# Performance work log

Measured on AMD Instinct MI355X. Metric: run time of the kernel, lower is better.

Reference implementation:

```python
import jax, jax.numpy as jnp
import numpy as np


def conv1x1(x, w, b):
    # x: [B,C,H,W], w: [O,C], b: [O]
    return jnp.einsum('bchw,oc->bohw', x, w) + b[None, :, None, None]


def dwconv(x, w):
    # depthwise conv, x: [B,C,H,W], w: [C,1,k,k], SAME padding (k odd, pad=k//2)
    return jax.lax.conv_general_dilated(
        x, w, window_strides=(1, 1), padding='SAME',
        dimension_numbers=('NCHW', 'OIHW', 'NCHW'),
        feature_group_count=x.shape[1])


def setup_inputs() -> dict:
    key = jax.random.key(0)
    ks = jax.random.split(key, 14)
    B, C, H, W = 16, 256, 64, 64
    OC = C // 16  # scale=16 -> 16
    WSCALE = 0.05
    r = lambda k, shape: jax.random.normal(k, shape, dtype=jnp.float32) * WSCALE
    return {
        'x': jax.random.normal(ks[0], (B, C, H, W), dtype=jnp.float32),
        'conv_w': r(ks[1], (C + 4, C)),           # 1x1 conv -> ctx (C) + gates (3+1)
        'conv_b': r(ks[2], (C + 4,)),
        'fw3': r(ks[3], (C, 1, 3, 3)),            # depthwise focal kernels
        'fw5': r(ks[4], (C, 1, 5, 5)),
        'fw7': r(ks[5], (C, 1, 7, 7)),
        'key_w': r(ks[6], (1, C)),                # Conv_key 1x1
        'key_b': r(ks[7], (1,)),
        'v1_w': r(ks[8], (OC, C)),                # Conv_value first 1x1
        'v1_b': r(ks[9], (OC,)),
        'ln_w': jnp.ones((OC,), dtype=jnp.float32),
        'ln_b': jnp.zeros((OC,), dtype=jnp.float32),
        'v2_w': r(ks[10], (C, OC)),               # Conv_value second 1x1
        'v2_b': r(ks[11], (C,)),
    }


def reference(x, conv_w, conv_b, fw3, fw5, fw7, key_w, key_b,
              v1_w, v1_b, ln_w, ln_b, v2_w, v2_b):
    B, C, H, W = x.shape
    # _contextAggregation
    t = conv1x1(x, conv_w, conv_b)          # [B, C+4, H, W]
    ctx, gates = t[:, :C], t[:, C:]         # [B,C,H,W], [B,4,H,W]
    ctx_all = jnp.zeros_like(ctx)
    for l, fw in enumerate((fw3, fw5, fw7)):
        ctx = jax.nn.gelu(dwconv(ctx, fw), approximate=False)  # torch GELU = exact erf
        ctx_all = ctx_all + ctx * gates[:, l:l + 1]
    ctx_global = jnp.mean(ctx, axis=(2, 3), keepdims=True)     # AdaptiveAvgPool2d(1)
    ctx_all = ctx_all + ctx_global * gates[:, 3:4]
    # GC-style channel attention: softmax over spatial positions
    k = conv1x1(ctx_all, key_w, key_b).reshape(B, H * W)       # [B, HW]
    k = jax.nn.softmax(k, axis=1)
    q = ctx_all.reshape(B, C, H * W)
    qk = jnp.einsum('bcn,bn->bc', q, k)[:, :, None, None]      # [B,C,1,1]
    # Conv_value: 1x1 -> LayerNorm([OC,1,1]) -> ReLU -> 1x1
    v = conv1x1(qk, v1_w, v1_b)                                # [B,OC,1,1]
    mu = jnp.mean(v, axis=(1, 2, 3), keepdims=True)
    var = jnp.var(v, axis=(1, 2, 3), keepdims=True)
    v = (v - mu) * jax.lax.rsqrt(var + 1e-5)
    v = v * ln_w[None, :, None, None] + ln_b[None, :, None, None]
    v = jax.nn.relu(v)
    v = conv1x1(v, v2_w, v2_b)                                 # [B,C,1,1]
    return ctx_all + v
```

## Files before the change

kernel.cpp:

```cpp
#include <hip/hip_runtime.h>

#define DEVFN __device__ __forceinline__

constexpr int B  = 16;
constexpr int C  = 256;
constexpr int N  = 64 * 64;
constexpr int O1 = C + 4;

typedef __attribute__((ext_vector_type(8)))  short bf16x8;
typedef __attribute__((ext_vector_type(4)))  short bf16x4;
typedef __attribute__((ext_vector_type(16))) float f32x16;
typedef unsigned short ushort_t;

DEVFN short f2bf(float f){
  union { float f; unsigned u; } p; p.f = f;
  unsigned r = p.u + 0x7fffu + ((p.u >> 16) & 1u);
  return (short)(r >> 16);
}
DEVFN unsigned pack2(float lo, float hi){
  return (unsigned)(ushort_t)f2bf(lo) | ((unsigned)(ushort_t)f2bf(hi) << 16);
}
DEVFN float lo2f(unsigned u){ union{unsigned u; float f;} p; p.u = u << 16; return p.f; }
DEVFN float hi2f(unsigned u){ union{unsigned u; float f;} p; p.u = u & 0xffff0000u; return p.f; }
DEVFN float bf2f(ushort_t s){ union{unsigned u; float f;} p; p.u = (unsigned)s << 16; return p.f; }

DEVFN float gelu_fast(float x){
  float y = 1.5957691216f * fmaf(0.044715f * x * x, x, x);
  float s = __builtin_amdgcn_rcpf(1.0f + __expf(-y));
  return x * s;
}

__global__ __launch_bounds__(256)
void k_wbf(const float* __restrict__ w, ushort_t* __restrict__ wbf){
  int idx = blockIdx.x * 256 + threadIdx.x;
  int o = idx >> 8, cc = idx & 255;
  wbf[idx] = (o < O1) ? (ushort_t)f2bf(w[o * 256 + cc]) : (ushort_t)0;
}

__global__ __launch_bounds__(256, 3)
void k_conv1_mfma(const float* __restrict__ x, const ushort_t* __restrict__ wbf,
                  const float* __restrict__ bias, ushort_t* __restrict__ ctxb,
                  float* __restrict__ gates){
  __shared__ __align__(16) short wlds[8 * 320 * 8];
  __shared__ __align__(16) short xlds[8 * 64 * 8];
  __shared__ float sbias[320];
  const int tid  = threadIdx.x;
  const int wave = tid >> 6;
  const int lane = tid & 63;
  const int l31  = lane & 31;
  const int lhi  = lane >> 5;
  const int pg0  = blockIdx.x * 64;
  const int b    = pg0 >> 12;
  const int n0   = pg0 & 4095;
  const int nwv  = (wave & 1) * 32;
  const int mrow = wave >> 1;

  sbias[tid] = bias[tid];
  if(tid < 64) sbias[256 + tid] = (256 + tid < O1) ? bias[256 + tid] : 0.f;

  const float* xpb = x + (size_t)b * C * N + n0;

  f32x16 acc[5];
  #pragma unroll
  for(int t = 0; t < 5; t++)
    #pragma unroll
    for(int r = 0; r < 16; r++) acc[t][r] = 0.f;

  float xf[2][8];

  auto pfX = [&](int kc){
    #pragma unroll
    for(int p = 0; p < 2; p++){
      const int idx = p * 256 + tid;
      const int kg = idx >> 6, n = idx & 63;
      const float* xp = xpb + (size_t)(kc + kg * 8) * N + n;
      #pragma unroll
      for(int j = 0; j < 8; j++) xf[p][j] = xp[(size_t)j * N];
    }
  };
  auto stX = [&](){
    #pragma unroll
    for(int p = 0; p < 2; p++){
      const int idx = p * 256 + tid;
      const int kg = idx >> 6, n = idx & 63;
      uint4 v;
      v.x = pack2(xf[p][0], xf[p][1]); v.y = pack2(xf[p][2], xf[p][3]);
      v.z = pack2(xf[p][4], xf[p][5]); v.w = pack2(xf[p][6], xf[p][7]);
      *(uint4*)&xlds[(kg * 64 + n) * 8] = v;
    }
  };
  auto stW = [&](int kc){
    #pragma unroll
    for(int q = 0; q < 10; q++){
      const int pidx = q * 256 + tid;
      const int kg = pidx / 320;
      const int m  = pidx - kg * 320;
      uint4 v = *(const uint4*)(wbf + (size_t)m * 256 + kc + kg * 8);
      *(uint4*)&wlds[(kg * 320 + m) * 8] = v;
    }
  };
  auto mfmaC = [&](){
    #pragma unroll
    for(int ks = 0; ks < 4; ks++){
      const int kg = ks * 2 + lhi;
      bf16x8 bfr = *(const bf16x8*)&xlds[(kg * 64 + nwv + l31) * 8];
      #pragma unroll
      for(int t = 0; t < 5; t++){
        const int m0 = (mrow + 2 * t) * 32;
        bf16x8 af = *(const bf16x8*)&wlds[(kg * 320 + m0 + l31) * 8];
        acc[t] = __builtin_amdgcn_mfma_f32_32x32x16_bf16(af, bfr, acc[t], 0, 0, 0);
      }
    }
  };

  stW(0); pfX(0); stX();
  __syncthreads();
  pfX(64);
  mfmaC();
  __syncthreads();
  stW(64); stX();
  __syncthreads();
  pfX(128);
  mfmaC();
  __syncthreads();
  stW(128); stX();
  __syncthreads();
  pfX(192);
  mfmaC();
  __syncthreads();
  stW(192); stX();
  __syncthreads();
  mfmaC();

  const int n = n0 + nwv + l31;
  #pragma unroll
  for(int t = 0; t < 5; t++){
    const int mt = (mrow + 2 * t) * 32;
    #pragma unroll
    for(int r = 0; r < 16; r++){
      const int row = (r & 3) + 8 * (r >> 2) + 4 * lhi;
      const int o = mt + row;
      if(o >= O1) continue;
      const float v = acc[t][r] + sbias[o];
      if(o < 256)
        ctxb[((size_t)(b * 256 + o)) * N + n] = (ushort_t)f2bf(v);
      else
        gates[((size_t)(b * 4 + (o - 256))) * N + n] = v;
    }
  }
}

constexpr int SSTR = 72;

DEVFN void unpack16(const short* p, float* wnd){
  uint4 a = *(const uint4*)p;
  uint4 b = *(const uint4*)(p + 8);
  unsigned ua[8] = {a.x, a.y, a.z, a.w, b.x, b.y, b.z, b.w};
  #pragma unroll
  for(int d = 0; d < 8; d++){ wnd[2*d] = lo2f(ua[d]); wnd[2*d+1] = hi2f(ua[d]); }
}

template<int K>
DEVFN void dw_stage(const short* src, const float* __restrict__ fw, int c,
                    int h, int w0, float* val){
  constexpr int R = K / 2;
  float acc[8];
  #pragma unroll
  for(int i = 0; i < 8; i++) acc[i] = 0.f;
  #pragma unroll
  for(int ky = 0; ky < K; ky++){
    const int r = h + ky - R;
    if((unsigned)r < 64u){
      float wnd[16];
      unpack16(&src[r * SSTR + w0], wnd);
      #pragma unroll
      for(int kx = 0; kx < K; kx++){
        const float wv = fw[c * K * K + ky * K + kx];
        #pragma unroll
        for(int i = 0; i < 8; i++)
          acc[i] = fmaf(wnd[i + kx + 4 - R], wv, acc[i]);
      }
    }
  }
  #pragma unroll
  for(int i = 0; i < 8; i++) val[i] = gelu_fast(acc[i]);
}

DEVFN void store_row(short* dst, int h, int w0, const float* val){
  bf16x4 lo, hi;
  #pragma unroll
  for(int i = 0; i < 4; i++){ lo[i] = f2bf(val[i]); hi[i] = f2bf(val[i + 4]); }
  *(bf16x4*)&dst[h * SSTR + w0 + 4] = lo;
  *(bf16x4*)&dst[h * SSTR + w0 + 8] = hi;
}

__global__ __launch_bounds__(512, 8)
void k_dwchain(ushort_t* __restrict__ ctxb, const float* __restrict__ fw3,
               const float* __restrict__ fw5, const float* __restrict__ fw7,
               const float* __restrict__ gates){
  __shared__ __align__(16) short bufA[64 * SSTR];
  __shared__ __align__(16) short bufB[64 * SSTR];
  __shared__ float wred[8];
  const int tid = threadIdx.x;
  const int plane = blockIdx.x;
  const int b = plane >> 8;
  const int c = plane & 255;
  const int h  = tid >> 3;
  const int w0 = (tid & 7) * 8;
  const int nbase = h * 64 + w0;

  if(tid < 64){
    bf16x4 z = {0, 0, 0, 0};
    *(bf16x4*)&bufA[tid * SSTR] = z;  *(bf16x4*)&bufA[tid * SSTR + 68] = z;
    *(bf16x4*)&bufB[tid * SSTR] = z;  *(bf16x4*)&bufB[tid * SSTR + 68] = z;
  }
  {
    bf16x8 iv = *(const bf16x8*)((const short*)ctxb + (size_t)plane * N + tid * 8);
    bf16x4 lo, hi;
    #pragma unroll
    for(int j = 0; j < 4; j++){ lo[j] = iv[j]; hi[j] = iv[j + 4]; }
    *(bf16x4*)&bufA[h * SSTR + w0 + 4] = lo;
    *(bf16x4*)&bufA[h * SSTR + w0 + 8] = hi;
  }
  __syncthreads();

  float ctxp[8];
  #pragma unroll
  for(int i = 0; i < 8; i++) ctxp[i] = 0.f;
  float val[8];

  dw_stage<3>(bufA, fw3, c, h, w0, val);
  {
    const float* gp = gates + ((size_t)(b * 4 + 0)) * N + nbase;
    float4 ga = *(const float4*)gp, gb = *(const float4*)(gp + 4);
    ctxp[0] = fmaf(val[0], ga.x, ctxp[0]); ctxp[1] = fmaf(val[1], ga.y, ctxp[1]);
    ctxp[2] = fmaf(val[2], ga.z, ctxp[2]); ctxp[3] = fmaf(val[3], ga.w, ctxp[3]);
    ctxp[4] = fmaf(val[4], gb.x, ctxp[4]); ctxp[5] = fmaf(val[5], gb.y, ctxp[5]);
    ctxp[6] = fmaf(val[6], gb.z, ctxp[6]); ctxp[7] = fmaf(val[7], gb.w, ctxp[7]);
    store_row(bufB, h, w0, val);
  }
  __syncthreads();

  dw_stage<5>(bufB, fw5, c, h, w0, val);
  {
    const float* gp = gates + ((size_t)(b * 4 + 1)) * N + nbase;
    float4 ga = *(const float4*)gp, gb = *(const float4*)(gp + 4);
    ctxp[0] = fmaf(val[0], ga.x, ctxp[0]); ctxp[1] = fmaf(val[1], ga.y, ctxp[1]);
    ctxp[2] = fmaf(val[2], ga.z, ctxp[2]); ctxp[3] = fmaf(val[3], ga.w, ctxp[3]);
    ctxp[4] = fmaf(val[4], gb.x, ctxp[4]); ctxp[5] = fmaf(val[5], gb.y, ctxp[5]);
    ctxp[6] = fmaf(val[6], gb.z, ctxp[6]); ctxp[7] = fmaf(val[7], gb.w, ctxp[7]);
    store_row(bufA, h, w0, val);
  }
  __syncthreads();

  dw_stage<7>(bufA, fw7, c, h, w0, val);
  float lsum = 0.f;
  {
    const float* gp = gates + ((size_t)(b * 4 + 2)) * N + nbase;
    float4 ga = *(const float4*)gp, gb = *(const float4*)(gp + 4);
    ctxp[0] = fmaf(val[0], ga.x, ctxp[0]); ctxp[1] = fmaf(val[1], ga.y, ctxp[1]);
    ctxp[2] = fmaf(val[2], ga.z, ctxp[2]); ctxp[3] = fmaf(val[3], ga.w, ctxp[3]);
    ctxp[4] = fmaf(val[4], gb.x, ctxp[4]); ctxp[5] = fmaf(val[5], gb.y, ctxp[5]);
    ctxp[6] = fmaf(val[6], gb.z, ctxp[6]); ctxp[7] = fmaf(val[7], gb.w, ctxp[7]);
    #pragma unroll
    for(int i = 0; i < 8; i++) lsum += val[i];
  }
  #pragma unroll
  for(int off = 32; off > 0; off >>= 1) lsum += __shfl_xor(lsum, off, 64);
  if((tid & 63) == 0) wred[tid >> 6] = lsum;
  __syncthreads();
  float mean = 0.f;
  #pragma unroll
  for(int i = 0; i < 8; i++) mean += wred[i];
  mean *= (1.0f / 4096.0f);

  {
    const float* gp = gates + ((size_t)(b * 4 + 3)) * N + nbase;
    float4 ga = *(const float4*)gp, gb = *(const float4*)(gp + 4);
    bf16x8 ov;
    ov[0] = f2bf(fmaf(mean, ga.x, ctxp[0])); ov[1] = f2bf(fmaf(mean, ga.y, ctxp[1]));
    ov[2] = f2bf(fmaf(mean, ga.z, ctxp[2])); ov[3] = f2bf(fmaf(mean, ga.w, ctxp[3]));
    ov[4] = f2bf(fmaf(mean, gb.x, ctxp[4])); ov[5] = f2bf(fmaf(mean, gb.y, ctxp[5]));
    ov[6] = f2bf(fmaf(mean, gb.z, ctxp[6])); ov[7] = f2bf(fmaf(mean, gb.w, ctxp[7]));
    *(bf16x8*)((short*)ctxb + (size_t)plane * N + nbase) = ov;
  }
}

__global__ __launch_bounds__(256)
void k_logits(const ushort_t* __restrict__ P, const float* __restrict__ key_w,
              const float* __restrict__ key_b, float* __restrict__ logits){
  __shared__ float kw[256];
  __shared__ float part[512];
  int tid = threadIdx.x;
  kw[tid] = key_w[tid];
  __syncthreads();
  int b  = blockIdx.x >> 5;
  int n0 = (blockIdx.x & 31) * 128;
  int cpart = tid >> 6, pxp = tid & 63;
  const ushort_t* pp = P + ((size_t)(b * 256 + cpart * 64)) * N + n0 + pxp * 2;
  float a0 = 0.f, a1 = 0.f;
  #pragma unroll 8
  for(int c = 0; c < 64; c++){
    unsigned u = *(const unsigned*)(pp + (size_t)c * N);
    float kwv = kw[cpart * 64 + c];
    a0 = fmaf(lo2f(u), kwv, a0);
    a1 = fmaf(hi2f(u), kwv, a1);
  }
  part[cpart * 128 + pxp * 2]     = a0;
  part[cpart * 128 + pxp * 2 + 1] = a1;
  __syncthreads();
  if(tid < 128){
    float l = part[tid] + part[128 + tid] + part[256 + tid] + part[384 + tid];
    logits[b * N + n0 + tid] = l + key_b[0];
  }
}

__global__ __launch_bounds__(1024)
void k_softmax(float* __restrict__ kbuf){
  __shared__ float wred[16];
  int b = blockIdx.x, tid = threadIdx.x;
  const int wave = tid >> 6, lane = tid & 63;
  float v[4];
  float m = -1e30f;
  #pragma unroll
  for(int i = 0; i < 4; i++){
    v[i] = kbuf[b * N + tid + i * 1024];
    m = fmaxf(m, v[i]);
  }
  #pragma unroll
  for(int off = 32; off > 0; off >>= 1) m = fmaxf(m, __shfl_xor(m, off, 64));
  if(lane == 0) wred[wave] = m;
  __syncthreads();
  float mm = -1e30f;
  #pragma unroll
  for(int i = 0; i < 16; i++) mm = fmaxf(mm, wred[i]);
  __syncthreads();
  float s = 0.f;
  #pragma unroll
  for(int i = 0; i < 4; i++){ v[i] = __expf(v[i] - mm); s += v[i]; }
  #pragma unroll
  for(int off = 32; off > 0; off >>= 1) s += __shfl_xor(s, off, 64);
  if(lane == 0) wred[wave] = s;
  __syncthreads();
  float tot = 0.f;
  #pragma unroll
  for(int i = 0; i < 16; i++) tot += wred[i];
  float inv = 1.0f / tot;
  #pragma unroll
  for(int i = 0; i < 4; i++)
    kbuf[b * N + tid + i * 1024] = v[i] * inv;
}

__global__ __launch_bounds__(256)
void k_qk(const ushort_t* __restrict__ P, const float* __restrict__ kbuf,
          float* __restrict__ qk){
  __shared__ float red[256];
  int plane = blockIdx.x, tid = threadIdx.x;
  int b = plane >> 8;
  const unsigned* pp = (const unsigned*)(P + (size_t)plane * N);
  const float2* kp = (const float2*)(kbuf + b * N);
  float acc = 0.f;
  #pragma unroll
  for(int i = 0; i < 8; i++){
    int idx = tid + i * 256;
    unsigned u = pp[idx];
    float2 kk = kp[idx];
    acc = fmaf(lo2f(u), kk.x, acc);
    acc = fmaf(hi2f(u), kk.y, acc);
  }
  red[tid] = acc; __syncthreads();
  for(int s = 128; s > 0; s >>= 1){
    if(tid < s) red[tid] += red[tid + s];
    __syncthreads();
  }
  if(tid == 0) qk[plane] = red[0];
}

__global__ __launch_bounds__(256)
void k_v(const float* __restrict__ qk, const float* __restrict__ v1w,
         const float* __restrict__ v1b, const float* __restrict__ lnw,
         const float* __restrict__ lnb, const float* __restrict__ v2w,
         const float* __restrict__ v2b, float* __restrict__ vout){
  int b = blockIdx.x, tid = threadIdx.x;
  __shared__ float qs[256];
  __shared__ float part[256];
  __shared__ float v1s[16];
  __shared__ float vr[16];
  __shared__ float stats[2];
  qs[tid] = qk[b * 256 + tid];
  __syncthreads();
  int oc = tid >> 4, ln = tid & 15;
  float p = 0.f;
  #pragma unroll
  for(int j = 0; j < 16; j++){
    int cc = ln + j * 16;
    p = fmaf(v1w[oc * 256 + cc], qs[cc], p);
  }
  part[tid] = p;
  __syncthreads();
  if(tid < 16){
    float s = v1b[tid];
    for(int j = 0; j < 16; j++) s += part[tid * 16 + j];
    v1s[tid] = s;
  }
  __syncthreads();
  if(tid == 0){
    float mu = 0.f;
    for(int i = 0; i < 16; i++) mu += v1s[i];
    mu *= (1.f / 16.f);
    float var = 0.f;
    for(int i = 0; i < 16; i++){ float d = v1s[i] - mu; var += d * d; }
    var *= (1.f / 16.f);
    stats[0] = mu; stats[1] = rsqrtf(var + 1e-5f);
  }
  __syncthreads();
  if(tid < 16){
    float vv = (v1s[tid] - stats[0]) * stats[1] * lnw[tid] + lnb[tid];
    vr[tid] = fmaxf(vv, 0.f);
  }
  __syncthreads();
  float o = v2b[tid];
  #pragma unroll
  for(int j = 0; j < 16; j++) o = fmaf(v2w[tid * 16 + j], vr[j], o);
  vout[b * 256 + tid] = o;
}

__global__ __launch_bounds__(256)
void k_final(float* __restrict__ out, const ushort_t* __restrict__ ctxb,
             const float* __restrict__ vout){
  int idx8 = blockIdx.x * 256 + threadIdx.x;
  int plane = idx8 >> 9;
  int off = (idx8 & 511) * 8;
  bf16x8 v = *(const bf16x8*)((const short*)ctxb + (size_t)plane * N + off);
  float vv = vout[plane];
  float4 o0, o1;
  o0.x = bf2f((ushort_t)v[0]) + vv; o0.y = bf2f((ushort_t)v[1]) + vv;
  o0.z = bf2f((ushort_t)v[2]) + vv; o0.w = bf2f((ushort_t)v[3]) + vv;
  o1.x = bf2f((ushort_t)v[4]) + vv; o1.y = bf2f((ushort_t)v[5]) + vv;
  o1.z = bf2f((ushort_t)v[6]) + vv; o1.w = bf2f((ushort_t)v[7]) + vv;
  float* op = out + (size_t)plane * N + off;
  *(float4*)op = o0;
  *(float4*)(op + 4) = o1;
}

extern "C" void kernel_launch(void* const* d_in, const int* in_sizes, int n_in,
                              void* d_out, int out_size, void* d_ws, size_t ws_size,
                              hipStream_t stream){
  const float* x      = (const float*)d_in[0];
  const float* conv_w = (const float*)d_in[1];
  const float* conv_b = (const float*)d_in[2];
  const float* fw3    = (const float*)d_in[3];
  const float* fw5    = (const float*)d_in[4];
  const float* fw7    = (const float*)d_in[5];
  const float* key_w  = (const float*)d_in[6];
  const float* key_b  = (const float*)d_in[7];
  const float* v1_w   = (const float*)d_in[8];
  const float* v1_b   = (const float*)d_in[9];
  const float* ln_w   = (const float*)d_in[10];
  const float* ln_b   = (const float*)d_in[11];
  const float* v2_w   = (const float*)d_in[12];
  const float* v2_b   = (const float*)d_in[13];
  float* out = (float*)d_out;

  const size_t PL = (size_t)B * C * N;
  char* p = (char*)d_ws;
  ushort_t* ctxb = (ushort_t*)p;  p += PL * sizeof(ushort_t);
  float* gates   = (float*)p;     p += (size_t)B * 4 * N * sizeof(float);
  float* kbuf    = (float*)p;     p += (size_t)B * N * sizeof(float);
  float* qkb     = (float*)p;     p += (size_t)B * C * sizeof(float);
  float* vout    = (float*)p;     p += (size_t)B * C * sizeof(float);
  ushort_t* wbf  = (ushort_t*)p;

  k_wbf<<<320, 256, 0, stream>>>(conv_w, wbf);
  k_conv1_mfma<<<1024, 256, 0, stream>>>(x, wbf, conv_b, ctxb, gates);
  k_dwchain<<<B * C, 512, 0, stream>>>(ctxb, fw3, fw5, fw7, gates);
  k_logits<<<512, 256, 0, stream>>>(ctxb, key_w, key_b, kbuf);
  k_softmax<<<B, 1024, 0, stream>>>(kbuf);
  k_qk<<<B * C, 256, 0, stream>>>(ctxb, kbuf, qkb);
  k_v<<<B, 256, 0, stream>>>(qkb, v1_w, v1_b, ln_w, ln_b, v2_w, v2_b, vout);
  k_final<<<8192, 256, 0, stream>>>(out, ctxb, vout);
}
```

Measured before the change: 287.0 us.

## Compute depthwise focal convs with packed fp16 dot2 on fp16 activations

The 1x1 conv now writes the ctx intermediate as fp16 instead of bf16, and the depthwise chain keeps its LDS stages in fp16. The depthwise windows are built from packed half pairs with alignbit shifts and reduced with v_dot2 against weights pre-packed into half2 by an extra block of the weight-conversion kernel. This roughly halves the FMA and unpack instruction count in the dominant depthwise kernel. GELU also switches to a single exp2 form. The cost is fp16 range and rounding risk on intermediates, plus a slightly different GELU approximation.

```diff
diff --git a/kernel.cpp b/kernel.cpp
--- a/kernel.cpp
+++ b/kernel.cpp
@@ -10,7 +10,9 @@
 typedef __attribute__((ext_vector_type(8)))  short bf16x8;
 typedef __attribute__((ext_vector_type(4)))  short bf16x4;
 typedef __attribute__((ext_vector_type(16))) float f32x16;
+typedef __attribute__((ext_vector_type(2)))  _Float16 h2;
 typedef unsigned short ushort_t;
+typedef unsigned int   uint32;
 
 DEVFN short f2bf(float f){
   union { float f; unsigned u; } p; p.f = f;
@@ -25,13 +27,58 @@
 DEVFN float bf2f(ushort_t s){ union{unsigned u; float f;} p; p.u = (unsigned)s << 16; return p.f; }
 
 DEVFN float gelu_fast(float x){
-  float y = 1.5957691216f * fmaf(0.044715f * x * x, x, x);
-  float s = __builtin_amdgcn_rcpf(1.0f + __expf(-y));
-  return x * s;
+  float s = x * x;
+  float t = x * fmaf(s, 0.1029432f, 2.3022082f);
+  float e = __builtin_amdgcn_exp2f(-t);
+  return x * __builtin_amdgcn_rcpf(1.0f + e);
+}
+
+DEVFN float fdot2f(uint32 a, uint32 b, float c){
+#if __has_builtin(__builtin_amdgcn_fdot2)
+  return __builtin_amdgcn_fdot2(__builtin_bit_cast(h2, a),
+                                __builtin_bit_cast(h2, b), c, false);
+#else
+  h2 ha = __builtin_bit_cast(h2, a), hb = __builtin_bit_cast(h2, b);
+  return fmaf((float)ha.x, (float)hb.x, fmaf((float)ha.y, (float)hb.y, c));
+#endif
+}
+
+DEVFN uint32 pkh(float a, float b){
+  _Float16 ha = (_Float16)a, hb = (_Float16)b;
+  return (uint32)__builtin_bit_cast(ushort_t, ha) |
+         ((uint32)__builtin_bit_cast(ushort_t, hb) << 16);
 }
 
 __global__ __launch_bounds__(256)
-void k_wbf(const float* __restrict__ w, ushort_t* __restrict__ wbf){
+void k_wbf(const float* __restrict__ w, ushort_t* __restrict__ wbf,
+           const float* __restrict__ fw3, const float* __restrict__ fw5,
+           const float* __restrict__ fw7, uint32* __restrict__ w3p,
+           uint32* __restrict__ w5p, uint32* __restrict__ w7p){
+  if(blockIdx.x == 320){
+    const int c = threadIdx.x;
+    #pragma unroll
+    for(int ky = 0; ky < 3; ky++){
+      const float* wr = fw3 + c * 9 + ky * 3;
+      w3p[c * 6 + ky * 2 + 0] = pkh(wr[0], wr[1]);
+      w3p[c * 6 + ky * 2 + 1] = pkh(wr[2], 0.f);
+    }
+    #pragma unroll
+    for(int ky = 0; ky < 5; ky++){
+      const float* wr = fw5 + c * 25 + ky * 5;
+      w5p[c * 15 + ky * 3 + 0] = pkh(wr[0], wr[1]);
+      w5p[c * 15 + ky * 3 + 1] = pkh(wr[2], wr[3]);
+      w5p[c * 15 + ky * 3 + 2] = pkh(wr[4], 0.f);
+    }
+    #pragma unroll
+    for(int ky = 0; ky < 7; ky++){
+      const float* wr = fw7 + c * 49 + ky * 7;
+      w7p[c * 28 + ky * 4 + 0] = pkh(wr[0], wr[1]);
+      w7p[c * 28 + ky * 4 + 1] = pkh(wr[2], wr[3]);
+      w7p[c * 28 + ky * 4 + 2] = pkh(wr[4], wr[5]);
+      w7p[c * 28 + ky * 4 + 3] = pkh(wr[6], 0.f);
+    }
+    return;
+  }
   int idx = blockIdx.x * 256 + threadIdx.x;
   int o = idx >> 8, cc = idx & 255;
   wbf[idx] = (o < O1) ? (ushort_t)f2bf(w[o * 256 + cc]) : (ushort_t)0;
@@ -142,43 +189,52 @@
       const int o = mt + row;
       if(o >= O1) continue;
       const float v = acc[t][r] + sbias[o];
-      if(o < 256)
-        ctxb[((size_t)(b * 256 + o)) * N + n] = (ushort_t)f2bf(v);
-      else
+      if(o < 256){
+        _Float16 hv = (_Float16)v;
+        ctxb[((size_t)(b * 256 + o)) * N + n] = __builtin_bit_cast(ushort_t, hv);
+      } else {
         gates[((size_t)(b * 4 + (o - 256))) * N + n] = v;
+      }
     }
   }
 }
 
 constexpr int SSTR = 72;
 
-DEVFN void unpack16(const short* p, float* wnd){
-  uint4 a = *(const uint4*)p;
-  uint4 b = *(const uint4*)(p + 8);
-  unsigned ua[8] = {a.x, a.y, a.z, a.w, b.x, b.y, b.z, b.w};
-  #pragma unroll
-  for(int d = 0; d < 8; d++){ wnd[2*d] = lo2f(ua[d]); wnd[2*d+1] = hi2f(ua[d]); }
-}
-
 template<int K>
-DEVFN void dw_stage(const short* src, const float* __restrict__ fw, int c,
-                    int h, int w0, float* val){
+DEVFN void dw_stage_dot(const short* src, const uint32* __restrict__ wp,
+                        int h, int w0, float* val){
   constexpr int R = K / 2;
+  constexpr int PAIRS = (K + 2) / 2;
   float acc[8];
   #pragma unroll
   for(int i = 0; i < 8; i++) acc[i] = 0.f;
   #pragma unroll
   for(int ky = 0; ky < K; ky++){
+    uint32 wk[PAIRS];
+    #pragma unroll
+    for(int t = 0; t < PAIRS; t++) wk[t] = wp[ky * PAIRS + t];
     const int r = h + ky - R;
     if((unsigned)r < 64u){
-      float wnd[16];
-      unpack16(&src[r * SSTR + w0], wnd);
+      const short* rp = &src[r * SSTR + w0];
+      uint4 a0 = *(const uint4*)rp;
+      uint4 a1 = *(const uint4*)(rp + 8);
+      uint32 P[8] = {a0.x, a0.y, a0.z, a0.w, a1.x, a1.y, a1.z, a1.w};
+      uint32 S[7];
       #pragma unroll
-      for(int kx = 0; kx < K; kx++){
-        const float wv = fw[c * K * K + ky * K + kx];
+      for(int j = 0; j < 7; j++)
+        S[j] = __builtin_amdgcn_alignbit(P[j + 1], P[j], 16);
+      #pragma unroll
+      for(int i = 0; i < 8; i++){
+        int j0, useP;
+        if      (K == 7){ useP =  (i & 1); j0 = (i + 1) >> 1; }
+        else if (K == 5){ useP = !(i & 1); j0 = (i >> 1) + 1; }
+        else            { useP =  (i & 1); j0 = (i >> 1) + ((i & 1) ? 2 : 1); }
         #pragma unroll
-        for(int i = 0; i < 8; i++)
-          acc[i] = fmaf(wnd[i + kx + 4 - R], wv, acc[i]);
+        for(int t = 0; t < PAIRS; t++){
+          const uint32 a = useP ? P[j0 + t] : S[j0 + t];
+          acc[i] = fdot2f(a, wk[t], acc[i]);
+        }
       }
     }
   }
@@ -186,17 +242,20 @@
   for(int i = 0; i < 8; i++) val[i] = gelu_fast(acc[i]);
 }
 
-DEVFN void store_row(short* dst, int h, int w0, const float* val){
-  bf16x4 lo, hi;
-  #pragma unroll
-  for(int i = 0; i < 4; i++){ lo[i] = f2bf(val[i]); hi[i] = f2bf(val[i + 4]); }
-  *(bf16x4*)&dst[h * SSTR + w0 + 4] = lo;
-  *(bf16x4*)&dst[h * SSTR + w0 + 8] = hi;
+DEVFN void store_row_h(short* dst, int h, int w0, const float* val){
+  uint32 o0 = __builtin_bit_cast(uint32, __builtin_amdgcn_cvt_pkrtz(val[0], val[1]));
+  uint32 o1 = __builtin_bit_cast(uint32, __builtin_amdgcn_cvt_pkrtz(val[2], val[3]));
+  uint32 o2 = __builtin_bit_cast(uint32, __builtin_amdgcn_cvt_pkrtz(val[4], val[5]));
+  uint32 o3 = __builtin_bit_cast(uint32, __builtin_amdgcn_cvt_pkrtz(val[6], val[7]));
+  uint2 t0; t0.x = o0; t0.y = o1;
+  uint2 t1; t1.x = o2; t1.y = o3;
+  *(uint2*)&dst[h * SSTR + w0 + 4] = t0;
+  *(uint2*)&dst[h * SSTR + w0 + 8] = t1;
 }
 
 __global__ __launch_bounds__(512, 8)
-void k_dwchain(ushort_t* __restrict__ ctxb, const float* __restrict__ fw3,
-               const float* __restrict__ fw5, const float* __restrict__ fw7,
+void k_dwchain(ushort_t* __restrict__ ctxb, const uint32* __restrict__ w3p,
+               const uint32* __restrict__ w5p, const uint32* __restrict__ w7p,
                const float* __restrict__ gates){
   __shared__ __align__(16) short bufA[64 * SSTR];
   __shared__ __align__(16) short bufB[64 * SSTR];
@@ -215,12 +274,11 @@
     *(bf16x4*)&bufB[tid * SSTR] = z;  *(bf16x4*)&bufB[tid * SSTR + 68] = z;
   }
   {
-    bf16x8 iv = *(const bf16x8*)((const short*)ctxb + (size_t)plane * N + tid * 8);
-    bf16x4 lo, hi;
-    #pragma unroll
-    for(int j = 0; j < 4; j++){ lo[j] = iv[j]; hi[j] = iv[j + 4]; }
-    *(bf16x4*)&bufA[h * SSTR + w0 + 4] = lo;
-    *(bf16x4*)&bufA[h * SSTR + w0 + 8] = hi;
+    const uint4 iv = *(const uint4*)((const short*)ctxb + (size_t)plane * N + tid * 8);
+    uint2 t0; t0.x = iv.x; t0.y = iv.y;
+    uint2 t1; t1.x = iv.z; t1.y = iv.w;
+    *(uint2*)&bufA[h * SSTR + w0 + 4] = t0;
+    *(uint2*)&bufA[h * SSTR + w0 + 8] = t1;
   }
   __syncthreads();
 
@@ -229,7 +287,7 @@
   for(int i = 0; i < 8; i++) ctxp[i] = 0.f;
   float val[8];
 
-  dw_stage<3>(bufA, fw3, c, h, w0, val);
+  dw_stage_dot<3>(bufA, w3p + c * 6, h, w0, val);
   {
     const float* gp = gates + ((size_t)(b * 4 + 0)) * N + nbase;
     float4 ga = *(const float4*)gp, gb = *(const float4*)(gp + 4);
@@ -237,11 +295,11 @@
     ctxp[2] = fmaf(val[2], ga.z, ctxp[2]); ctxp[3] = fmaf(val[3], ga.w, ctxp[3]);
     ctxp[4] = fmaf(val[4], gb.x, ctxp[4]); ctxp[5] = fmaf(val[5], gb.y, ctxp[5]);
     ctxp[6] = fmaf(val[6], gb.z, ctxp[6]); ctxp[7] = fmaf(val[7], gb.w, ctxp[7]);
-    store_row(bufB, h, w0, val);
-  }
-  __syncthreads();
-
-  dw_stage<5>(bufB, fw5, c, h, w0, val);
+    store_row_h(bufB, h, w0, val);
+  }
+  __syncthreads();
+
+  dw_stage_dot<5>(bufB, w5p + c * 15, h, w0, val);
   {
     const float* gp = gates + ((size_t)(b * 4 + 1)) * N + nbase;
     float4 ga = *(const float4*)gp, gb = *(const float4*)(gp + 4);
@@ -249,11 +307,11 @@
     ctxp[2] = fmaf(val[2], ga.z, ctxp[2]); ctxp[3] = fmaf(val[3], ga.w, ctxp[3]);
     ctxp[4] = fmaf(val[4], gb.x, ctxp[4]); ctxp[5] = fmaf(val[5], gb.y, ctxp[5]);
     ctxp[6] = fmaf(val[6], gb.z, ctxp[6]); ctxp[7] = fmaf(val[7], gb.w, ctxp[7]);
-    store_row(bufA, h, w0, val);
-  }
-  __syncthreads();
-
-  dw_stage<7>(bufA, fw7, c, h, w0, val);
+    store_row_h(bufA, h, w0, val);
+  }
+  __syncthreads();
+
+  dw_stage_dot<7>(bufA, w7p + c * 28, h, w0, val);
   float lsum = 0.f;
   {
     const float* gp = gates + ((size_t)(b * 4 + 2)) * N + nbase;
@@ -469,11 +527,14 @@
   float* kbuf    = (float*)p;     p += (size_t)B * N * sizeof(float);
   float* qkb     = (float*)p;     p += (size_t)B * C * sizeof(float);
   float* vout    = (float*)p;     p += (size_t)B * C * sizeof(float);
-  ushort_t* wbf  = (ushort_t*)p;
-
-  k_wbf<<<320, 256, 0, stream>>>(conv_w, wbf);
+  ushort_t* wbf  = (ushort_t*)p;  p += (size_t)320 * 256 * sizeof(ushort_t);
+  uint32* w3p    = (uint32*)p;    p += (size_t)256 * 6 * sizeof(uint32);
+  uint32* w5p    = (uint32*)p;    p += (size_t)256 * 15 * sizeof(uint32);
+  uint32* w7p    = (uint32*)p;
+
+  k_wbf<<<321, 256, 0, stream>>>(conv_w, wbf, fw3, fw5, fw7, w3p, w5p, w7p);
   k_conv1_mfma<<<1024, 256, 0, stream>>>(x, wbf, conv_b, ctxb, gates);
-  k_dwchain<<<B * C, 512, 0, stream>>>(ctxb, fw3, fw5, fw7, gates);
+  k_dwchain<<<B * C, 512, 0, stream>>>(ctxb, w3p, w5p, w7p, gates);
   k_logits<<<512, 256, 0, stream>>>(ctxb, key_w, key_b, kbuf);
   k_softmax<<<B, 1024, 0, stream>>>(kbuf);
   k_qk<<<B * C, 256, 0, stream>>>(ctxb, kbuf, qkb);
```

Measured after the change: 270.8 us. 1.06x faster.
